# Kernel optimization log

Measured on AMD Instinct MI355X. Metric: run time of the kernel, lower is better.

## Reference

```python
import jax, jax.numpy as jnp
import numpy as np

THIRD = 1.0 / 3.0


def setup_inputs() -> dict:
    key = jax.random.key(0)
    obs = jax.random.uniform(key, (8192, 64, 16), dtype=jnp.float32)
    ego_init = jnp.array([0.0, 1.0], dtype=jnp.float32)
    other_init = jnp.array([1.0, 0.0], dtype=jnp.float32)
    return {"obs": obs, "ego_init": ego_init, "other_init": other_init}


def _build_edges(obs):
    """Fixed-shape jax version of get_edge_index + unique + remove_self_loops.
    Returns [2, B*10*(N-1)] int32, lexicographically sorted unique directed edges,
    padded with -1 at the end (variable-length output is expressed via padding)."""
    B, N, _ = obs.shape
    M = B * N          # total node count
    SENT = M           # sentinel id, sorts after all valid ids
    Xs = obs[:, :, 0]
    Ys = obs[:, :, 1]

    def per_batch(xs, ys):
        order = jnp.argsort(xs)            # stable sort by x-position
        ysort = ys[order]
        m0 = (ysort <= THIRD) & (ysort > 0.0)
        m1 = (ysort > THIRD) & (ysort <= 2.0 * THIRD)
        m2 = (ysort >= 2.0 * THIRD) & (ysort < 1.0)
        masks = jnp.stack([m0, m1, m2, m0 | m1, m1 | m2])  # [5, N]

        def chain(m):
            # stable sort puts lane members first, preserving x-order
            g = order[jnp.argsort((~m).astype(jnp.int32))]   # [N]
            cnt = jnp.sum(m)
            valid = jnp.arange(N - 1) < (cnt - 1)
            a = jnp.where(valid, g[:-1], N)   # local sentinel = N
            b = jnp.where(valid, g[1:], N)
            # bidirectional consecutive-neighbor edges, [2, 2*(N-1)]
            return jnp.stack([jnp.concatenate([a, b]), jnp.concatenate([b, a])])

        e = jax.vmap(chain)(masks)               # [5, 2, 2*(N-1)]
        return e.transpose(1, 0, 2).reshape(2, -1)  # [2, 10*(N-1)]

    edges = jax.vmap(per_batch)(Xs, Ys)          # [B, 2, 10*(N-1)]
    offs = (jnp.arange(B) * N)[:, None, None]
    edges = jnp.where(edges == N, SENT, edges + offs)

    src = edges[:, 0, :].reshape(-1)
    dst = edges[:, 1, :].reshape(-1)
    bad = (src == dst) | (src >= M)              # self-loops / padding -> sentinel
    src = jnp.where(bad, SENT, src)
    dst = jnp.where(bad, SENT, dst)

    # unique(edge_index, axis=1): lexsort, mark dups, push dups to the end
    idx = jnp.lexsort((dst, src))
    s, d = src[idx], dst[idx]
    dup = (s == jnp.roll(s, 1)) & (d == jnp.roll(d, 1))
    dup = dup.at[0].set(False)
    s = jnp.where(dup, SENT, s)
    d = jnp.where(dup, SENT, d)
    idx2 = jnp.lexsort((d, s))
    s, d = s[idx2], d[idx2]
    pad = s >= M
    return jnp.stack([jnp.where(pad, -1, s), jnp.where(pad, -1, d)]).astype(jnp.int32)


def reference(obs, ego_init, other_init):
    B, N, D = obs.shape
    # node features: obs concat with ego/other one-hot init flag
    init = jnp.where(jnp.arange(N)[:, None] == 0, ego_init[None, :], other_init[None, :])  # [N, 2]
    x = jnp.concatenate([obs, jnp.broadcast_to(init, (B, N, init.shape[-1]))], axis=-1)
    x = x.reshape(B * N, D + init.shape[-1])
    edge_index = _build_edges(obs)
    return x, edge_index
```

## Files before the change

### kernel.cpp

```cpp
#include <hip/hip_runtime.h>
#include <cstdint>
#include <cstddef>

#define NAGENT 64
#define WPB 4
#define ROWS_K1 128
#define CAP 640
#define SLOT_PB 630

__global__ __launch_bounds__(256) void concat_kernel(
    const float4* __restrict__ obs4, const float* __restrict__ ego,
    const float* __restrict__ oth, float4* __restrict__ out4,
    float* __restrict__ xy)
{
    __shared__ float buf[ROWS_K1 * 16];
    const int t = threadIdx.x;
    const int R0 = blockIdx.x * ROWS_K1;

    const float4* src = obs4 + (size_t)R0 * 4;
    ((float4*)buf)[t]       = src[t];
    ((float4*)buf)[t + 256] = src[t + 256];
    const float e0 = ego[0], e1 = ego[1];
    const float o0 = oth[0], o1 = oth[1];
    __syncthreads();

    float4* dst = out4 + (size_t)blockIdx.x * 576;
    #pragma unroll
    for (int k = 0; k < 3; ++k) {
        const int f = t + k * 256;
        if (f >= 576) break;
        float4 v;
        float* vp = (float*)&v;
        #pragma unroll
        for (int c = 0; c < 4; ++c) {
            const unsigned g   = (unsigned)(f * 4 + c);
            const unsigned row = g / 18u;
            const unsigned col = g - row * 18u;
            float val;
            if (col < 16u) {
                val = buf[row * 16u + col];
                if (col < 2u) xy[((size_t)R0 + row) * 2u + col] = val;
            } else {
                const bool egorow = ((row & 63u) == 0u);
                val = (col == 16u) ? (egorow ? e0 : o0) : (egorow ? e1 : o1);
            }
            vp[c] = val;
        }
        dst[f] = v;
    }
}

__global__ __launch_bounds__(64 * WPB) void build_kernel(
    const float2* __restrict__ xy, unsigned int* __restrict__ adj_g,
    int* __restrict__ counts, int B)
{
    const int wave = threadIdx.x >> 6;
    const int lane = threadIdx.x & 63;
    const int b = blockIdx.x * WPB + wave;

    __shared__ int   order_s[WPB][NAGENT];
    __shared__ float ys_s[WPB][NAGENT];
    __shared__ unsigned int adj_s[WPB][NAGENT][2];

    const float2 p = xy[(size_t)b * NAGENT + lane];
    const float x = p.x;
    const float y = p.y;

    int rank = 0;
    #pragma unroll 8
    for (int j = 0; j < 64; ++j) {
        float xj = __shfl(x, j);
        rank += (xj < x || (xj == x && j < lane)) ? 1 : 0;
    }
    order_s[wave][rank] = lane;
    ys_s[wave][lane] = y;
    adj_s[wave][lane][0] = 0u;
    adj_s[wave][lane][1] = 0u;
    __syncthreads();

    const int a = order_s[wave][lane];
    const float ya = ys_s[wave][a];
    const float T1 = 1.0f / 3.0f;
    const float T2 = 2.0f / 3.0f;
    const bool m0 = (ya <= T1) && (ya > 0.0f);
    const bool m1 = (ya > T1) && (ya <= T2);
    const bool m2 = (ya >= T2) && (ya < 1.0f);
    bool ms[5];
    ms[0] = m0; ms[1] = m1; ms[2] = m2; ms[3] = m0 || m1; ms[4] = m1 || m2;

    #pragma unroll
    for (int k = 0; k < 5; ++k) {
        unsigned long long bits = __ballot(ms[k]);
        unsigned long long higher = (lane == 63) ? 0ULL : (bits >> (lane + 1));
        if (ms[k] && higher != 0ULL) {
            int q = lane + 1 + __builtin_ctzll(higher);
            int bb = order_s[wave][q];
            atomicOr(&adj_s[wave][a][bb >> 5], 1u << (bb & 31));
            atomicOr(&adj_s[wave][bb][a >> 5], 1u << (a & 31));
        }
    }
    __syncthreads();

    const unsigned int r0 = adj_s[wave][lane][0];
    const unsigned int r1 = adj_s[wave][lane][1];
    adj_g[(size_t)b * 128 + 2 * lane + 0] = r0;
    adj_g[(size_t)b * 128 + 2 * lane + 1] = r1;

    int c = __popc(r0) + __popc(r1);
    #pragma unroll
    for (int off = 1; off < 64; off <<= 1) {
        int t = __shfl_up(c, off);
        if (lane >= off) c += t;
    }
    if (lane == 63) counts[b] = c;
}

__global__ __launch_bounds__(64 * WPB) void emit_kernel(
    const unsigned int* __restrict__ adj_g, const int* __restrict__ counts,
    float* __restrict__ out_es, float* __restrict__ out_ed, int B, int slots)
{
    __shared__ float es_s[WPB][CAP];
    __shared__ float ed_s[WPB][CAP];
    const int wave = threadIdx.x >> 6;
    const int lane = threadIdx.x & 63;
    const int b = blockIdx.x * WPB + wave;

    int pre = 0, tot = 0;
    for (int i = lane; i < B; i += 64) {
        const int v = counts[i];
        tot += v;
        pre += (i < b) ? v : 0;
    }
    #pragma unroll
    for (int off = 32; off >= 1; off >>= 1) {
        pre += __shfl_xor(pre, off);
        tot += __shfl_xor(tot, off);
    }
    const int cnt = counts[b];
    const int suf = tot - pre - cnt;

    unsigned int r0 = adj_g[(size_t)b * 128 + 2 * lane + 0];
    unsigned int r1 = adj_g[(size_t)b * 128 + 2 * lane + 1];
    const int c = __popc(r0) + __popc(r1);
    int inc = c;
    #pragma unroll
    for (int off = 1; off < 64; off <<= 1) {
        int t = __shfl_up(inc, off);
        if (lane >= off) inc += t;
    }
    int pos = inc - c;
    const int gbase = b * NAGENT;
    const float sg = (float)(gbase + lane);
    while (r0) {
        int d = __builtin_ctz(r0); r0 &= r0 - 1u;
        es_s[wave][pos] = sg; ed_s[wave][pos] = (float)(gbase + d); ++pos;
    }
    while (r1) {
        int d = 32 + __builtin_ctz(r1); r1 &= r1 - 1u;
        es_s[wave][pos] = sg; ed_s[wave][pos] = (float)(gbase + d); ++pos;
    }
    __syncthreads();

    for (int j = lane; j < cnt; j += 64) {
        out_es[pre + j] = es_s[wave][j];
        out_ed[pre + j] = ed_s[wave][j];
    }
    const int D = SLOT_PB - cnt;
    const int X = SLOT_PB * (B - 1 - b) - suf;
    const int pbeg = slots - X - D;
    for (int j = lane; j < D; j += 64) {
        out_es[pbeg + j] = -1.0f;
        out_ed[pbeg + j] = -1.0f;
    }
}

extern "C" void kernel_launch(void* const* d_in, const int* in_sizes, int n_in,
                              void* d_out, int out_size, void* d_ws, size_t ws_size,
                              hipStream_t stream)
{
    const float* obs = (const float*)d_in[0];
    const float* ego = (const float*)d_in[1];
    const float* oth = (const float*)d_in[2];

    const int B = in_sizes[0] / (NAGENT * 16);
    const int M = B * NAGENT;
    const int xtotal = M * 18;
    const int slots = B * SLOT_PB;

    float* out_x  = (float*)d_out;
    float* out_es = out_x + xtotal;
    float* out_ed = out_es + slots;

    float*        xy     = (float*)d_ws;
    unsigned int* adj_g  = (unsigned int*)(xy + (size_t)2 * M);
    int*          counts = (int*)(adj_g + (size_t)B * 128);

    concat_kernel<<<M / ROWS_K1, 256, 0, stream>>>(
        (const float4*)obs, ego, oth, (float4*)d_out, xy);
    build_kernel<<<B / WPB, 64 * WPB, 0, stream>>>(
        (const float2*)xy, adj_g, counts, B);
    emit_kernel<<<B / WPB, 64 * WPB, 0, stream>>>(
        adj_g, counts, out_es, out_ed, B, slots);
}
```

Before: 138.9 us.

## Fuse concat and edge-build kernels, vectorize edge stores and count reads

Merges the concat kernel and the build kernel into one launch. Each block now loads 256 rows (four batches) and keeps x/y positions in shared memory, so the xy workspace round-trip and one kernel launch are removed. The emit kernel reads counts as int4, stores the adjacency as uint2, and writes edges and the -1 padding with aligned float4 stores plus scalar head and tail loops. This adds shared-memory use per block and halves the block count of the concat stage.

```diff
diff --git a/kernel.cpp b/kernel.cpp
--- a/kernel.cpp
+++ b/kernel.cpp
@@ -4,31 +4,44 @@
 
 #define NAGENT 64
 #define WPB 4
-#define ROWS_K1 128
+#define ROWS_A 256
 #define CAP 640
 #define SLOT_PB 630
 
-__global__ __launch_bounds__(256) void concat_kernel(
+__global__ __launch_bounds__(256) void concat_build_kernel(
     const float4* __restrict__ obs4, const float* __restrict__ ego,
     const float* __restrict__ oth, float4* __restrict__ out4,
-    float* __restrict__ xy)
+    uint2* __restrict__ adj_g, int* __restrict__ counts)
 {
-    __shared__ float buf[ROWS_K1 * 16];
+    __shared__ float  buf[ROWS_A * 16];
+    __shared__ float2 xy_s[ROWS_A];
+    __shared__ int    order_s[WPB][NAGENT];
+    __shared__ unsigned int adj_s[WPB][NAGENT][2];
+
     const int t = threadIdx.x;
-    const int R0 = blockIdx.x * ROWS_K1;
-
-    const float4* src = obs4 + (size_t)R0 * 4;
-    ((float4*)buf)[t]       = src[t];
-    ((float4*)buf)[t + 256] = src[t + 256];
+    const int wave = t >> 6;
+    const int lane = t & 63;
+
+    adj_s[wave][lane][0] = 0u;
+    adj_s[wave][lane][1] = 0u;
+
+    const float4* src = obs4 + (size_t)blockIdx.x * (ROWS_A * 4);
+    #pragma unroll
+    for (int k = 0; k < 4; ++k) {
+        const int f = t + k * 256;
+        float4 v = src[f];
+        ((float4*)buf)[f] = v;
+        if ((f & 3) == 0) xy_s[f >> 2] = make_float2(v.x, v.y);
+    }
     const float e0 = ego[0], e1 = ego[1];
     const float o0 = oth[0], o1 = oth[1];
     __syncthreads();
 
-    float4* dst = out4 + (size_t)blockIdx.x * 576;
-    #pragma unroll
-    for (int k = 0; k < 3; ++k) {
+    float4* dst = out4 + (size_t)blockIdx.x * (ROWS_A * 18 / 4);
+    #pragma unroll
+    for (int k = 0; k < 5; ++k) {
         const int f = t + k * 256;
-        if (f >= 576) break;
+        if (f >= ROWS_A * 18 / 4) break;
         float4 v;
         float* vp = (float*)&v;
         #pragma unroll
@@ -39,32 +52,18 @@
             float val;
             if (col < 16u) {
                 val = buf[row * 16u + col];
-                if (col < 2u) xy[((size_t)R0 + row) * 2u + col] = val;
             } else {
-                const bool egorow = ((row & 63u) == 0u);
-                val = (col == 16u) ? (egorow ? e0 : o0) : (egorow ? e1 : o1);
+                const bool eg = ((row & 63u) == 0u);
+                val = (col == 16u) ? (eg ? e0 : o0) : (eg ? e1 : o1);
             }
             vp[c] = val;
         }
         dst[f] = v;
     }
-}
-
-__global__ __launch_bounds__(64 * WPB) void build_kernel(
-    const float2* __restrict__ xy, unsigned int* __restrict__ adj_g,
-    int* __restrict__ counts, int B)
-{
-    const int wave = threadIdx.x >> 6;
-    const int lane = threadIdx.x & 63;
+
     const int b = blockIdx.x * WPB + wave;
-
-    __shared__ int   order_s[WPB][NAGENT];
-    __shared__ float ys_s[WPB][NAGENT];
-    __shared__ unsigned int adj_s[WPB][NAGENT][2];
-
-    const float2 p = xy[(size_t)b * NAGENT + lane];
+    const float2 p = xy_s[wave * 64 + lane];
     const float x = p.x;
-    const float y = p.y;
 
     int rank = 0;
     #pragma unroll 8
@@ -73,13 +72,10 @@
         rank += (xj < x || (xj == x && j < lane)) ? 1 : 0;
     }
     order_s[wave][rank] = lane;
-    ys_s[wave][lane] = y;
-    adj_s[wave][lane][0] = 0u;
-    adj_s[wave][lane][1] = 0u;
     __syncthreads();
 
     const int a = order_s[wave][lane];
-    const float ya = ys_s[wave][a];
+    const float ya = xy_s[wave * 64 + a].y;
     const float T1 = 1.0f / 3.0f;
     const float T2 = 2.0f / 3.0f;
     const bool m0 = (ya <= T1) && (ya > 0.0f);
@@ -103,20 +99,16 @@
 
     const unsigned int r0 = adj_s[wave][lane][0];
     const unsigned int r1 = adj_s[wave][lane][1];
-    adj_g[(size_t)b * 128 + 2 * lane + 0] = r0;
-    adj_g[(size_t)b * 128 + 2 * lane + 1] = r1;
+    adj_g[(size_t)b * NAGENT + lane] = make_uint2(r0, r1);
 
     int c = __popc(r0) + __popc(r1);
     #pragma unroll
-    for (int off = 1; off < 64; off <<= 1) {
-        int t = __shfl_up(c, off);
-        if (lane >= off) c += t;
-    }
-    if (lane == 63) counts[b] = c;
+    for (int off = 32; off >= 1; off >>= 1) c += __shfl_xor(c, off);
+    if (lane == 0) counts[b] = c;
 }
 
 __global__ __launch_bounds__(64 * WPB) void emit_kernel(
-    const unsigned int* __restrict__ adj_g, const int* __restrict__ counts,
+    const uint2* __restrict__ adj_g, const int* __restrict__ counts,
     float* __restrict__ out_es, float* __restrict__ out_ed, int B, int slots)
 {
     __shared__ float es_s[WPB][CAP];
@@ -126,10 +118,13 @@
     const int b = blockIdx.x * WPB + wave;
 
     int pre = 0, tot = 0;
-    for (int i = lane; i < B; i += 64) {
-        const int v = counts[i];
-        tot += v;
-        pre += (i < b) ? v : 0;
+    const int4* c4 = (const int4*)counts;
+    for (int i = lane; i < B / 4; i += 64) {
+        const int4 v = c4[i];
+        const int base = 4 * i;
+        tot += v.x + v.y + v.z + v.w;
+        pre += ((base + 0 < b) ? v.x : 0) + ((base + 1 < b) ? v.y : 0)
+             + ((base + 2 < b) ? v.z : 0) + ((base + 3 < b) ? v.w : 0);
     }
     #pragma unroll
     for (int off = 32; off >= 1; off >>= 1) {
@@ -139,8 +134,8 @@
     const int cnt = counts[b];
     const int suf = tot - pre - cnt;
 
-    unsigned int r0 = adj_g[(size_t)b * 128 + 2 * lane + 0];
-    unsigned int r1 = adj_g[(size_t)b * 128 + 2 * lane + 1];
+    const uint2 ar = adj_g[(size_t)b * NAGENT + lane];
+    unsigned int r0 = ar.x, r1 = ar.y;
     const int c = __popc(r0) + __popc(r1);
     int inc = c;
     #pragma unroll
@@ -161,16 +156,54 @@
     }
     __syncthreads();
 
-    for (int j = lane; j < cnt; j += 64) {
-        out_es[pre + j] = es_s[wave][j];
-        out_ed[pre + j] = ed_s[wave][j];
-    }
-    const int D = SLOT_PB - cnt;
-    const int X = SLOT_PB * (B - 1 - b) - suf;
-    const int pbeg = slots - X - D;
-    for (int j = lane; j < D; j += 64) {
-        out_es[pbeg + j] = -1.0f;
-        out_ed[pbeg + j] = -1.0f;
+    {
+        int h = (4 - (pre & 3)) & 3;
+        if (h > cnt) h = cnt;
+        for (int j = lane; j < h; j += 64) {
+            out_es[pre + j] = es_s[wave][j];
+            out_ed[pre + j] = ed_s[wave][j];
+        }
+        const int body = (cnt - h) >> 2;
+        float4* oes4 = (float4*)(out_es + pre + h);
+        float4* oed4 = (float4*)(out_ed + pre + h);
+        for (int q = lane; q < body; q += 64) {
+            const int j = h + 4 * q;
+            float4 v, w;
+            v.x = es_s[wave][j];     w.x = ed_s[wave][j];
+            v.y = es_s[wave][j + 1]; w.y = ed_s[wave][j + 1];
+            v.z = es_s[wave][j + 2]; w.z = ed_s[wave][j + 2];
+            v.w = es_s[wave][j + 3]; w.w = ed_s[wave][j + 3];
+            oes4[q] = v;
+            oed4[q] = w;
+        }
+        for (int j = h + 4 * body + lane; j < cnt; j += 64) {
+            out_es[pre + j] = es_s[wave][j];
+            out_ed[pre + j] = ed_s[wave][j];
+        }
+    }
+
+    {
+        const int D = SLOT_PB - cnt;
+        const int X = SLOT_PB * (B - 1 - b) - suf;
+        const int pbeg = slots - X - D;
+        int h = (4 - (pbeg & 3)) & 3;
+        if (h > D) h = D;
+        for (int j = lane; j < h; j += 64) {
+            out_es[pbeg + j] = -1.0f;
+            out_ed[pbeg + j] = -1.0f;
+        }
+        const int body = (D - h) >> 2;
+        float4* oes4 = (float4*)(out_es + pbeg + h);
+        float4* oed4 = (float4*)(out_ed + pbeg + h);
+        const float4 neg1 = make_float4(-1.0f, -1.0f, -1.0f, -1.0f);
+        for (int q = lane; q < body; q += 64) {
+            oes4[q] = neg1;
+            oed4[q] = neg1;
+        }
+        for (int j = h + 4 * body + lane; j < D; j += 64) {
+            out_es[pbeg + j] = -1.0f;
+            out_ed[pbeg + j] = -1.0f;
+        }
     }
 }
 
@@ -191,14 +224,11 @@
     float* out_es = out_x + xtotal;
     float* out_ed = out_es + slots;
 
-    float*        xy     = (float*)d_ws;
-    unsigned int* adj_g  = (unsigned int*)(xy + (size_t)2 * M);
-    int*          counts = (int*)(adj_g + (size_t)B * 128);
-
-    concat_kernel<<<M / ROWS_K1, 256, 0, stream>>>(
-        (const float4*)obs, ego, oth, (float4*)d_out, xy);
-    build_kernel<<<B / WPB, 64 * WPB, 0, stream>>>(
-        (const float2*)xy, adj_g, counts, B);
+    uint2* adj_g  = (uint2*)d_ws;
+    int*   counts = (int*)(adj_g + (size_t)B * NAGENT);
+
+    concat_build_kernel<<<M / ROWS_A, 256, 0, stream>>>(
+        (const float4*)obs, ego, oth, (float4*)d_out, adj_g, counts);
     emit_kernel<<<B / WPB, 64 * WPB, 0, stream>>>(
         adj_g, counts, out_es, out_ed, B, slots);
 }
```

Result: faster. 124.8 us (-10.1%).
